# Kernel optimization log

Hardware: AMD Instinct MI355X
Metric: run time of the kernel (lower is better)

## Reference

```python
import jax, jax.numpy as jnp
import numpy as np

B, C, H, W = 2, 128, 64, 64
D_STATE, D_CONV, EXPAND = 16, 4, 2
D_INNER = EXPAND * C
DT_RANK = (C + 15) // 16  # ceil(d_model/16) = 8


def layernorm(x, w, b):
    # WithBias_LayerNorm over last (channel) dim, unbiased=False variance
    mu = jnp.mean(x, axis=-1, keepdims=True)
    var = jnp.mean((x - mu) ** 2, axis=-1, keepdims=True)
    return (x - mu) / jnp.sqrt(var + 1e-5) * w + b


def causal_conv1d_silu(x, w, b):
    # x: (b, d, l); w: (d, k) depthwise; causal pad k-1 on left, then SiLU
    k = w.shape[1]
    out = jax.lax.conv_general_dilated(
        x, w[:, None, :], window_strides=(1,), padding=[(k - 1, 0)],
        dimension_numbers=('NCH', 'OIH', 'NCH'), feature_group_count=w.shape[0])
    return jax.nn.silu(out + b[:, None])


def selective_scan(dA, dBu, Cm):
    # dA, dBu: (b, d, l, n); Cm: (b, n, l) -> y: (b, d, l)
    dA_t = jnp.moveaxis(dA, 2, 0)    # (l, b, d, n)
    dBu_t = jnp.moveaxis(dBu, 2, 0)  # (l, b, d, n)
    C_t = jnp.moveaxis(Cm, 2, 0)     # (l, b, n)

    def step(h, inp):
        a, bu, c = inp
        h = a * h + bu
        y = jnp.einsum('bdn,bn->bd', h, c)
        return h, y

    h0 = jnp.zeros(dA.shape[:2] + (dA.shape[3],), dA.dtype)
    _, ys = jax.lax.scan(step, h0, (dA_t, dBu_t, C_t))
    return jnp.moveaxis(ys, 0, 2)  # (b, d, l)


def mamba_branch(x3, W_in, W_z, conv_w, conv_b, W_x, W_dt, b_dt, A, D, W_out):
    # x3: (b, l, d_model) normalized input
    x = jnp.einsum('bld,ed->bel', x3, W_in)  # (b, d_inner, l)
    z = jnp.einsum('bld,ed->bel', x3, W_z)
    x = causal_conv1d_silu(x, conv_w, conv_b)
    xdbl = jnp.einsum('bdl,ed->bel', x, W_x)  # (b, dt_rank+2n, l)
    dt_low = xdbl[:, :DT_RANK]
    Bm = xdbl[:, DT_RANK:DT_RANK + D_STATE]
    Cm = xdbl[:, DT_RANK + D_STATE:]
    delta = jax.nn.softplus(jnp.einsum('brl,dr->bdl', dt_low, W_dt) + b_dt[:, None])
    dA = jnp.exp(delta[:, :, :, None] * A[None, :, None, :])           # (b,d,l,n)
    dBu = jnp.einsum('bdl,bnl->bdln', delta * x, Bm)                    # (b,d,l,n)
    y = selective_scan(dA, dBu, Cm)
    y = y + D[:, None] * x
    y = y * jax.nn.silu(z)
    return jnp.einsum('bdl,od->blo', y, W_out)  # (b, l, d_model)


def setup_inputs() -> dict:
    key = jax.random.key(0)
    ks = jax.random.split(key, 24)
    rn = lambda k, shp, s: jax.random.normal(k, shp, dtype=jnp.float32) * s
    inp = {}
    inp['pan'] = rn(ks[0], (B, C, H, W), 1.0)
    inp['ms'] = rn(ks[1], (B, C, H, W), 1.0)
    inp['norm_w_pan'] = jnp.ones((C,), jnp.float32)
    inp['norm_b_pan'] = jnp.zeros((C,), jnp.float32)
    inp['norm_w_ms'] = jnp.ones((C,), jnp.float32)
    inp['norm_b_ms'] = jnp.zeros((C,), jnp.float32)
    inp['W_in_pan'] = rn(ks[2], (D_INNER, C), C ** -0.5)
    inp['W_in_ms'] = rn(ks[3], (D_INNER, C), C ** -0.5)
    inp['W_z_pan'] = rn(ks[4], (D_INNER, C), C ** -0.5)
    inp['W_z_ms'] = rn(ks[5], (D_INNER, C), C ** -0.5)
    inp['conv_w_pan'] = rn(ks[6], (D_INNER, D_CONV), D_CONV ** -0.5)
    inp['conv_b_pan'] = rn(ks[7], (D_INNER,), 0.02)
    inp['conv_w_ms'] = rn(ks[8], (D_INNER, D_CONV), D_CONV ** -0.5)
    inp['conv_b_ms'] = rn(ks[9], (D_INNER,), 0.02)
    inp['W_x_pan'] = rn(ks[10], (DT_RANK + 2 * D_STATE, D_INNER), D_INNER ** -0.5)
    inp['W_x_ms'] = rn(ks[11], (DT_RANK + 2 * D_STATE, D_INNER), D_INNER ** -0.5)
    dt_std = DT_RANK ** -0.5
    inp['W_dt_pan'] = jax.random.uniform(ks[12], (D_INNER, DT_RANK), jnp.float32, -dt_std, dt_std)
    inp['W_dt_ms'] = jax.random.uniform(ks[13], (D_INNER, DT_RANK), jnp.float32, -dt_std, dt_std)
    # dt bias init: inverse-softplus of dt ~ logU[1e-3, 1e-1]
    u = np.asarray(jax.random.uniform(ks[14], (D_INNER,)))
    dt = np.exp(u * (np.log(0.1) - np.log(0.001)) + np.log(0.001)).clip(min=1e-4)
    inv_dt = dt + np.log(-np.expm1(-dt))
    inp['b_dt_pan'] = jnp.asarray(inv_dt, jnp.float32)
    inp['b_dt_ms'] = jnp.asarray(inv_dt, jnp.float32)
    inp['A_log'] = jnp.log(jnp.broadcast_to(jnp.arange(1, D_STATE + 1, dtype=jnp.float32), (D_INNER, D_STATE)))
    inp['D_pan'] = jnp.ones((D_INNER,), jnp.float32)
    inp['D_ms'] = jnp.ones((D_INNER,), jnp.float32)
    inp['W_out_pan'] = rn(ks[15], (C, D_INNER), D_INNER ** -0.5)
    inp['W_out_ms'] = rn(ks[16], (C, D_INNER), D_INNER ** -0.5)
    return inp


def reference(pan, ms, norm_w_pan, norm_b_pan, norm_w_ms, norm_b_ms,
              W_in_pan, W_in_ms, W_z_pan, W_z_ms,
              conv_w_pan, conv_b_pan, conv_w_ms, conv_b_ms,
              W_x_pan, W_x_ms, W_dt_pan, W_dt_ms, b_dt_pan, b_dt_ms,
              A_log, D_pan, D_ms, W_out_pan, W_out_ms):
    b, c, h, w = pan.shape
    A = -jnp.exp(A_log)
    pan3 = layernorm(pan.reshape(b, c, h * w).transpose(0, 2, 1), norm_w_pan, norm_b_pan)
    ms3 = layernorm(ms.reshape(b, c, h * w).transpose(0, 2, 1), norm_w_ms, norm_b_ms)
    out_pan = mamba_branch(pan3, W_in_pan, W_z_pan, conv_w_pan, conv_b_pan,
                           W_x_pan, W_dt_pan, b_dt_pan, A, D_pan, W_out_pan)
    out_ms = mamba_branch(ms3, W_in_ms, W_z_ms, conv_w_ms, conv_b_ms,
                          W_x_ms, W_dt_ms, b_dt_ms, A, D_ms, W_out_ms)
    out_pan = out_pan.transpose(0, 2, 1).reshape(b, c, h, w)
    out_ms = out_ms.transpose(0, 2, 1).reshape(b, c, h, w)
    return (out_pan, out_ms)
```

## Files before the change

### kernel.cpp

```cpp
#include <hip/hip_runtime.h>
#include <hip/hip_bf16.h>

constexpr int BB = 2;
constexpr int CC = 128;
constexpr int LL = 4096;
constexpr int DI = 256;
constexpr int DS = 16;
constexpr int DR = 8;
constexpr int DX = 40;
constexpr int NZ = 2 * BB;
constexpr int CH = 8;
constexpr int NCH = LL / CH;
constexpr int SEG = 32;

typedef short bf16x8 __attribute__((ext_vector_type(8)));
typedef float f32x4 __attribute__((ext_vector_type(4)));
typedef float f32x2 __attribute__((ext_vector_type(2)));

__device__ __forceinline__ unsigned short f2bf(float x) {
    __hip_bfloat16 h = __float2bfloat16(x);
    return *(unsigned short*)&h;
}
__device__ __forceinline__ float bflo(unsigned u) { return __uint_as_float(u << 16); }
__device__ __forceinline__ float bfhi(unsigned u) { return __uint_as_float(u & 0xffff0000u); }
__device__ __forceinline__ float bfu(unsigned short u) { return __uint_as_float((unsigned)u << 16); }
__device__ __forceinline__ float fast_rcp(float x) { return __builtin_amdgcn_rcpf(x); }
__device__ __forceinline__ float siluf(float x) { return x * fast_rcp(1.f + __expf(-x)); }
__device__ __forceinline__ float softplusf(float x) {
    const float z = exp2f(x * 1.44269504f);
    return (x > 20.f) ? x : 0.69314718f * log2f(1.f + z);
}

__global__ __launch_bounds__(256) void prep_kernel(
    const float* __restrict__ pan, const float* __restrict__ ms,
    const float* __restrict__ wpan, const float* __restrict__ bpan,
    const float* __restrict__ wms, const float* __restrict__ bms,
    const float* __restrict__ Winp, const float* __restrict__ Winm,
    const float* __restrict__ Wzp, const float* __restrict__ Wzm,
    const float* __restrict__ Woutp, const float* __restrict__ Woutm,
    const float* __restrict__ Wxp, const float* __restrict__ Wxm,
    unsigned short* __restrict__ x3b, unsigned short* __restrict__ wb)
{
    const int bx = blockIdx.x;
    const int t = threadIdx.x;
    if (bx >= 256) {
        const int i = (bx - 256) * 256 + t;
        const float* src; int off;
        if (i < 32768)       { src = Winp;  off = i; }
        else if (i < 65536)  { src = Winm;  off = i - 32768; }
        else if (i < 98304)  { src = Wzp;   off = i - 65536; }
        else if (i < 131072) { src = Wzm;   off = i - 98304; }
        else if (i < 163840) { src = Woutp; off = i - 131072; }
        else if (i < 196608) { src = Woutm; off = i - 163840; }
        else if (i < 206848) { src = Wxp;   off = i - 196608; }
        else                 { src = Wxm;   off = i - 206848; }
        wb[i] = f2bf(src[off]);
        return;
    }
    const int zi = bx >> 6;
    const int br = zi >> 1, b = zi & 1;
    const float* inp = br ? ms : pan;
    const float* wp = br ? wms : wpan;
    const float* bp = br ? bms : bpan;
    const int l0 = (bx & 63) * 64;
    const int lo = t & 63, c4 = t >> 6;
    const float* base = inp + (size_t)b * CC * LL + l0 + lo;
    float vals[32];
    float s = 0.f, s2 = 0.f;
    #pragma unroll
    for (int i = 0; i < 32; i++) {
        const int c = c4 * 32 + i;
        const float v = base[(size_t)c * LL];
        vals[i] = v; s += v; s2 += v * v;
    }
    __shared__ float red[2][4][64];
    red[0][c4][lo] = s; red[1][c4][lo] = s2;
    __syncthreads();
    const float S  = red[0][0][lo] + red[0][1][lo] + red[0][2][lo] + red[0][3][lo];
    const float S2 = red[1][0][lo] + red[1][1][lo] + red[1][2][lo] + red[1][3][lo];
    const float mu = S * (1.f / CC);
    const float var = S2 * (1.f / CC) - mu * mu;
    const float rstd = rsqrtf(var + 1e-5f);
    unsigned short* out = x3b + (size_t)zi * CC * LL + l0 + lo;
    #pragma unroll
    for (int i = 0; i < 32; i++) {
        const int c = c4 * 32 + i;
        out[(size_t)c * LL] = f2bf((vals[i] - mu) * rstd * wp[c] + bp[c]);
    }
}

__global__ __launch_bounds__(256) void gemm_inz_mfma(
    const unsigned short* __restrict__ wb, const unsigned short* __restrict__ x3b,
    unsigned short* __restrict__ xpre16, unsigned short* __restrict__ zb16)
{
    const int zi = blockIdx.z;
    const int my = blockIdx.y;
    const unsigned short* WI = wb + (zi >= BB ? 32768 : 0);
    const unsigned short* WZ = WI + 65536;
    const int mbase = my * 64;
    const unsigned short* Xb = x3b + (size_t)zi * CC * LL;
    const int n0 = blockIdx.x * 64;
    const int t = threadIdx.x;
    const int w = t >> 6, ln = t & 63;
    const int nf = ln & 15, qb = ln >> 4;
    bf16x8 afragI[4], afragZ[4];
    const int mrow = mbase + w * 16 + nf;
    #pragma unroll
    for (int c = 0; c < 4; c++) {
        afragI[c] = *(const bf16x8*)(WI + (size_t)mrow * CC + c * 32 + qb * 8);
        afragZ[c] = *(const bf16x8*)(WZ + (size_t)mrow * CC + c * 32 + qb * 8);
    }
    __shared__ unsigned short Bs[64][40];
    unsigned* Bw = (unsigned*)Bs;
    f32x4 accI[4] = {}, accZ[4] = {};
    const int kp = t >> 4, n4 = (t & 15) * 4;
    ushort4 a0 = *(const ushort4*)(Xb + (size_t)(2 * kp) * LL + n0 + n4);
    ushort4 a1 = *(const ushort4*)(Xb + (size_t)(2 * kp + 1) * LL + n0 + n4);
    #pragma unroll
    for (int kc = 0; kc < 4; kc++) {
        if (kc) __syncthreads();
        Bw[(n4 + 0) * 20 + kp] = (unsigned)a0.x | ((unsigned)a1.x << 16);
        Bw[(n4 + 1) * 20 + kp] = (unsigned)a0.y | ((unsigned)a1.y << 16);
        Bw[(n4 + 2) * 20 + kp] = (unsigned)a0.z | ((unsigned)a1.z << 16);
        Bw[(n4 + 3) * 20 + kp] = (unsigned)a0.w | ((unsigned)a1.w << 16);
        __syncthreads();
        if (kc < 3) {
            a0 = *(const ushort4*)(Xb + (size_t)((kc + 1) * 32 + 2 * kp) * LL + n0 + n4);
            a1 = *(const ushort4*)(Xb + (size_t)((kc + 1) * 32 + 2 * kp + 1) * LL + n0 + n4);
        }
        #pragma unroll
        for (int ns = 0; ns < 4; ns++) {
            const bf16x8 bf = *(const bf16x8*)(&Bs[ns * 16 + nf][qb * 8]);
            accI[ns] = __builtin_amdgcn_mfma_f32_16x16x32_bf16(afragI[kc], bf, accI[ns], 0, 0, 0);
            accZ[ns] = __builtin_amdgcn_mfma_f32_16x16x32_bf16(afragZ[kc], bf, accZ[ns], 0, 0, 0);
        }
    }
    #pragma unroll
    for (int ns = 0; ns < 4; ns++)
        #pragma unroll
        for (int r = 0; r < 4; r++) {
            const int m = mbase + w * 16 + qb * 4 + r;
            xpre16[((size_t)zi * DI + m) * LL + n0 + ns * 16 + nf] = f2bf(accI[ns][r]);
            zb16  [((size_t)zi * DI + m) * LL + n0 + ns * 16 + nf] = f2bf(accZ[ns][r]);
        }
}

__global__ __launch_bounds__(256) void gemm_x_mfma(
    const unsigned short* __restrict__ wb, const unsigned short* __restrict__ xpre16,
    const float* __restrict__ cw0, const float* __restrict__ cb0,
    const float* __restrict__ cw1, const float* __restrict__ cb1,
    unsigned short* __restrict__ xc, unsigned short* __restrict__ xdbl16)
{
    const int zi = blockIdx.z;
    const unsigned short* W = wb + 196608 + (zi >= BB ? 10240 : 0);
    const float* cw = (zi >= BB) ? cw1 : cw0;
    const float* cb = (zi >= BB) ? cb1 : cb0;
    const unsigned short* Xb = xpre16 + (size_t)zi * DI * LL;
    unsigned short* xcb = xc + (size_t)zi * DI * LL;
    const int n0 = blockIdx.x * 64;
    const int t = threadIdx.x;
    const int w = t >> 6, ln = t & 63;
    const int nf = ln & 15, qb = ln >> 4;
    bf16x8 zfrag;
    #pragma unroll
    for (int j = 0; j < 8; j++) zfrag[j] = 0;
    bf16x8 afrag[8];
    const int mrow = w * 16 + nf;
    #pragma unroll
    for (int c = 0; c < 8; c++)
        afrag[c] = (mrow < DX) ? *(const bf16x8*)(W + (size_t)mrow * DI + c * 32 + qb * 8) : zfrag;
    __shared__ unsigned short Bs[64][40];
    unsigned* Bw = (unsigned*)Bs;
    f32x4 acc[4] = {};
    const int kp = t >> 4, n4 = (t & 15) * 4;
    const bool edge = (n0 + n4 == 0);
    ushort4 cur0, cur1, prv0, prv1;
    {
        const unsigned short* xp0 = Xb + (size_t)(2 * kp) * LL + n0 + n4;
        const unsigned short* xp1 = Xb + (size_t)(2 * kp + 1) * LL + n0 + n4;
        cur0 = *(const ushort4*)xp0; cur1 = *(const ushort4*)xp1;
        if (!edge) { prv0 = *(const ushort4*)(xp0 - 4); prv1 = *(const ushort4*)(xp1 - 4); }
        else { prv0 = ushort4{0,0,0,0}; prv1 = ushort4{0,0,0,0}; }
    }
    #pragma unroll
    for (int kc = 0; kc < 8; kc++) {
        ushort4 o[2];
        #pragma unroll
        for (int rr = 0; rr < 2; rr++) {
            const int e = kc * 32 + 2 * kp + rr;
            const ushort4 cur = rr ? cur1 : cur0;
            const ushort4 prv = rr ? prv1 : prv0;
            const float xm3 = bfu(prv.y), xm2 = bfu(prv.z), xm1 = bfu(prv.w);
            const float c0 = bfu(cur.x), c1 = bfu(cur.y);
            const float c2 = bfu(cur.z), c3 = bfu(cur.w);
            const float w0 = cw[e * 4 + 0], w1 = cw[e * 4 + 1];
            const float w2 = cw[e * 4 + 2], w3 = cw[e * 4 + 3];
            const float bias = cb[e];
            o[rr].x = f2bf(siluf(w0 * xm3 + w1 * xm2 + w2 * xm1 + w3 * c0 + bias));
            o[rr].y = f2bf(siluf(w0 * xm2 + w1 * xm1 + w2 * c0 + w3 * c1 + bias));
            o[rr].z = f2bf(siluf(w0 * xm1 + w1 * c0 + w2 * c1 + w3 * c2 + bias));
            o[rr].w = f2bf(siluf(w0 * c0 + w1 * c1 + w2 * c2 + w3 * c3 + bias));
        }
        *(ushort4*)(xcb + (size_t)(kc * 32 + 2 * kp) * LL + n0 + n4) = o[0];
        *(ushort4*)(xcb + (size_t)(kc * 32 + 2 * kp + 1) * LL + n0 + n4) = o[1];
        if (kc) __syncthreads();
        Bw[(n4 + 0) * 20 + kp] = (unsigned)(unsigned short)o[0].x | ((unsigned)(unsigned short)o[1].x << 16);
        Bw[(n4 + 1) * 20 + kp] = (unsigned)(unsigned short)o[0].y | ((unsigned)(unsigned short)o[1].y << 16);
        Bw[(n4 + 2) * 20 + kp] = (unsigned)(unsigned short)o[0].z | ((unsigned)(unsigned short)o[1].z << 16);
        Bw[(n4 + 3) * 20 + kp] = (unsigned)(unsigned short)o[0].w | ((unsigned)(unsigned short)o[1].w << 16);
        __syncthreads();
        if (kc < 7) {
            const unsigned short* xp0 = Xb + (size_t)((kc + 1) * 32 + 2 * kp) * LL + n0 + n4;
            const unsigned short* xp1 = Xb + (size_t)((kc + 1) * 32 + 2 * kp + 1) * LL + n0 + n4;
            cur0 = *(const ushort4*)xp0; cur1 = *(const ushort4*)xp1;
            if (!edge) { prv0 = *(const ushort4*)(xp0 - 4); prv1 = *(const ushort4*)(xp1 - 4); }
        }
        #pragma unroll
        for (int ns = 0; ns < 4; ns++) {
            const bf16x8 bf = *(const bf16x8*)(&Bs[ns * 16 + nf][qb * 8]);
            acc[ns] = __builtin_amdgcn_mfma_f32_16x16x32_bf16(afrag[kc], bf, acc[ns], 0, 0, 0);
        }
    }
    #pragma unroll
    for (int ns = 0; ns < 4; ns++)
        #pragma unroll
        for (int r = 0; r < 4; r++) {
            const int m = w * 16 + qb * 4 + r;
            if (m < DX)
                xdbl16[((size_t)zi * DX + m) * LL + n0 + ns * 16 + nf] = f2bf(acc[ns][r]);
        }
}

__global__ __launch_bounds__(256) void gemm_out_mfma(
    const unsigned short* __restrict__ wb, const unsigned short* __restrict__ yb,
    float* __restrict__ outg)
{
    const int zi = blockIdx.z;
    const unsigned short* W = wb + 131072 + (zi >= BB ? 32768 : 0);
    const int mbase = blockIdx.y * 64;
    const unsigned short* Xb = yb + (size_t)zi * DI * LL;
    const int n0 = blockIdx.x * 64;
    const int t = threadIdx.x;
    const int w = t >> 6, ln = t & 63;
    const int nf = ln & 15, qb = ln >> 4;
    bf16x8 afrag[8];
    const int mrow = mbase + w * 16 + nf;
    #pragma unroll
    for (int c = 0; c < 8; c++)
        afrag[c] = *(const bf16x8*)(W + (size_t)mrow * DI + c * 32 + qb * 8);
    __shared__ unsigned short Bs[64][40];
    unsigned* Bw = (unsigned*)Bs;
    f32x4 acc[4] = {};
    const int kp = t >> 4, n4 = (t & 15) * 4;
    ushort4 a0 = *(const ushort4*)(Xb + (size_t)(2 * kp) * LL + n0 + n4);
    ushort4 a1 = *(const ushort4*)(Xb + (size_t)(2 * kp + 1) * LL + n0 + n4);
    #pragma unroll
    for (int kc = 0; kc < 8; kc++) {
        if (kc) __syncthreads();
        Bw[(n4 + 0) * 20 + kp] = (unsigned)a0.x | ((unsigned)a1.x << 16);
        Bw[(n4 + 1) * 20 + kp] = (unsigned)a0.y | ((unsigned)a1.y << 16);
        Bw[(n4 + 2) * 20 + kp] = (unsigned)a0.z | ((unsigned)a1.z << 16);
        Bw[(n4 + 3) * 20 + kp] = (unsigned)a0.w | ((unsigned)a1.w << 16);
        __syncthreads();
        if (kc < 7) {
            a0 = *(const ushort4*)(Xb + (size_t)((kc + 1) * 32 + 2 * kp) * LL + n0 + n4);
            a1 = *(const ushort4*)(Xb + (size_t)((kc + 1) * 32 + 2 * kp + 1) * LL + n0 + n4);
        }
        #pragma unroll
        for (int ns = 0; ns < 4; ns++) {
            const bf16x8 bf = *(const bf16x8*)(&Bs[ns * 16 + nf][qb * 8]);
            acc[ns] = __builtin_amdgcn_mfma_f32_16x16x32_bf16(afrag[kc], bf, acc[ns], 0, 0, 0);
        }
    }
    #pragma unroll
    for (int ns = 0; ns < 4; ns++)
        #pragma unroll
        for (int r = 0; r < 4; r++) {
            const int m = mbase + w * 16 + qb * 4 + r;
            outg[((size_t)zi * CC + m) * LL + n0 + ns * 16 + nf] = acc[ns][r];
        }
}

__global__ __launch_bounds__(512, 8) void scan_fused(
    const unsigned short* __restrict__ xc, const unsigned short* __restrict__ xdbl16,
    const float* __restrict__ A_log,
    const float* __restrict__ Wdt0, const float* __restrict__ Wdt1,
    const float* __restrict__ bdt0, const float* __restrict__ bdt1,
    const float* __restrict__ D0, const float* __restrict__ D1,
    const unsigned short* __restrict__ zb16, unsigned short* __restrict__ yb)
{
    const int blk = blockIdx.x;
    const int zi = blk >> 8;
    const int d  = blk & (DI - 1);
    const int t = threadIdx.x;
    const int l0 = t * CH;
    __shared__ float Ssh[DS * (NCH + 1)];
    __shared__ float sdl_sh[NCH];
    __shared__ float Pseg[DS * (SEG + 1)];
    __shared__ float Sseg[DS * (SEG + 1)];
    const unsigned short* xdb = xdbl16 + (size_t)zi * DX * LL;
    const float* Wdt = (zi >= BB) ? Wdt1 : Wdt0;
    const float* bdt = (zi >= BB) ? bdt1 : bdt0;
    const float dbias = bdt[d];
    float rx[CH];
    {
        const uint4 xv4 = *(const uint4*)(xc + (size_t)blk * LL + l0);
        rx[0] = bflo(xv4.x); rx[1] = bfhi(xv4.x);
        rx[2] = bflo(xv4.y); rx[3] = bfhi(xv4.y);
        rx[4] = bflo(xv4.z); rx[5] = bfhi(xv4.z);
        rx[6] = bflo(xv4.w); rx[7] = bfhi(xv4.w);
    }
    float e[CH], rdlx[CH];
    {
        f32x2 acc2[4];
        #pragma unroll
        for (int j = 0; j < 4; j++) acc2[j] = f32x2{dbias, dbias};
        #pragma unroll
        for (int r = 0; r < DR; r++) {
            const float wr = Wdt[d * DR + r];
            const f32x2 w2 = {wr, wr};
            const uint4 v = *(const uint4*)(xdb + (size_t)r * LL + l0);
            acc2[0] = w2 * f32x2{bflo(v.x), bfhi(v.x)} + acc2[0];
            acc2[1] = w2 * f32x2{bflo(v.y), bfhi(v.y)} + acc2[1];
            acc2[2] = w2 * f32x2{bflo(v.z), bfhi(v.z)} + acc2[2];
            acc2[3] = w2 * f32x2{bflo(v.w), bfhi(v.w)} + acc2[3];
        }
        float av[CH];
        av[0] = acc2[0].x; av[1] = acc2[0].y; av[2] = acc2[1].x; av[3] = acc2[1].y;
        av[4] = acc2[2].x; av[5] = acc2[2].y; av[6] = acc2[3].x; av[7] = acc2[3].y;
        float sdl = 0.f;
        #pragma unroll
        for (int i = 0; i < CH; i++) {
            const float sp = softplusf(av[i]);
            sdl += sp;
            rdlx[i] = sp * rx[i];
            e[i] = __expf(-sp);
        }
        sdl_sh[t] = sdl;
    }
    bool fast = true;
    #pragma unroll
    for (int n = 0; n < DS; n++)
        fast = fast && (fabsf(__expf(A_log[d * DS + n]) - (float)(n + 1)) < 1e-3f);
    const unsigned short* Bbase = xdb + (size_t)DR * LL;
    const unsigned short* Cbase = Bbase + (size_t)DS * LL;
    float y[CH];
    const int n2 = t & 15, sg = t >> 4;

    if (fast) {
        f32x2 e2[4], rdlx2[4];
        #pragma unroll
        for (int j = 0; j < 4; j++) {
            e2[j] = f32x2{e[2 * j], e[2 * j + 1]};
            rdlx2[j] = f32x2{rdlx[2 * j], rdlx[2 * j + 1]};
        }
        f32x2 pw2[4];
        #pragma unroll
        for (int j = 0; j < 4; j++) pw2[j] = f32x2{1.f, 1.f};
        #pragma unroll 4
        for (int n = 0; n < DS; n++) {
            const uint4 bv = *(const uint4*)(Bbase + (size_t)n * LL + l0);
            const f32x2 b0 = {bflo(bv.x), bfhi(bv.x)};
            const f32x2 b1 = {bflo(bv.y), bfhi(bv.y)};
            const f32x2 b2 = {bflo(bv.z), bfhi(bv.z)};
            const f32x2 b3 = {bflo(bv.w), bfhi(bv.w)};
            pw2[0] *= e2[0]; pw2[1] *= e2[1]; pw2[2] *= e2[2]; pw2[3] *= e2[3];
            const f32x2 u0 = rdlx2[0] * b0, u1 = rdlx2[1] * b1;
            const f32x2 u2 = rdlx2[2] * b2, u3 = rdlx2[3] * b3;
            float hn = u0.x;
            hn = fmaf(pw2[0].y, hn, u0.y);
            hn = fmaf(pw2[1].x, hn, u1.x);
            hn = fmaf(pw2[1].y, hn, u1.y);
            hn = fmaf(pw2[2].x, hn, u2.x);
            hn = fmaf(pw2[2].y, hn, u2.y);
            hn = fmaf(pw2[3].x, hn, u3.x);
            hn = fmaf(pw2[3].y, hn, u3.y);
            Ssh[n * (NCH + 1) + t] = hn;
        }
        __syncthreads();
        {
            const float Ann = -(float)(n2 + 1);
            float P = 1.f, S = 0.f;
            #pragma unroll
            for (int k = 0; k < 16; k++) {
                const int c = sg * 16 + k;
                const float p = __expf(Ann * sdl_sh[c]);
                const float s = Ssh[n2 * (NCH + 1) + c];
                S = fmaf(p, S, s);
                P *= p;
            }
            Pseg[n2 * (SEG + 1) + sg] = P;
            Sseg[n2 * (SEG + 1) + sg] = S;
        }
        __syncthreads();
        if (t < DS) {
            float h = 0.f;
            #pragma unroll 4
            for (int c2 = 0; c2 < SEG; c2++) {
                const float p = Pseg[t * (SEG + 1) + c2];
                const float s = Sseg[t * (SEG + 1) + c2];
                Sseg[t * (SEG + 1) + c2] = h;
                h = fmaf(p, h, s);
            }
        }
        __syncthreads();
        {
            const float Ann = -(float)(n2 + 1);
            float h = Sseg[n2 * (SEG + 1) + sg];
            #pragma unroll
            for (int k = 0; k < 16; k++) {
                const int c = sg * 16 + k;
                const float p = __expf(Ann * sdl_sh[c]);
                const float s = Ssh[n2 * (NCH + 1) + c];
                Ssh[n2 * (NCH + 1) + c] = h;
                h = fmaf(p, h, s);
            }
        }
        __syncthreads();
        f32x2 y2[4];
        #pragma unroll
        for (int j = 0; j < 4; j++) { y2[j] = f32x2{0.f, 0.f}; pw2[j] = f32x2{1.f, 1.f}; }
        #pragma unroll 2
        for (int n = 0; n < DS; n++) {
            const uint4 bv = *(const uint4*)(Bbase + (size_t)n * LL + l0);
            const uint4 cv = *(const uint4*)(Cbase + (size_t)n * LL + l0);
            const f32x2 b0 = {bflo(bv.x), bfhi(bv.x)};
            const f32x2 b1 = {bflo(bv.y), bfhi(bv.y)};
            const f32x2 b2 = {bflo(bv.z), bfhi(bv.z)};
            const f32x2 b3 = {bflo(bv.w), bfhi(bv.w)};
            const f32x2 c0 = {bflo(cv.x), bfhi(cv.x)};
            const f32x2 c1 = {bflo(cv.y), bfhi(cv.y)};
            const f32x2 c2 = {bflo(cv.z), bfhi(cv.z)};
            const f32x2 c3 = {bflo(cv.w), bfhi(cv.w)};
            pw2[0] *= e2[0]; pw2[1] *= e2[1]; pw2[2] *= e2[2]; pw2[3] *= e2[3];
            const f32x2 u0 = rdlx2[0] * b0, u1 = rdlx2[1] * b1;
            const f32x2 u2 = rdlx2[2] * b2, u3 = rdlx2[3] * b3;
            const float hp = Ssh[n * (NCH + 1) + t];
            const float h0 = fmaf(pw2[0].x, hp, u0.x);
            const float h1 = fmaf(pw2[0].y, h0, u0.y);
            y2[0] = f32x2{h0, h1} * c0 + y2[0];
            const float h2 = fmaf(pw2[1].x, h1, u1.x);
            const float h3 = fmaf(pw2[1].y, h2, u1.y);
            y2[1] = f32x2{h2, h3} * c1 + y2[1];
            const float h4 = fmaf(pw2[2].x, h3, u2.x);
            const float h5 = fmaf(pw2[2].y, h4, u2.y);
            y2[2] = f32x2{h4, h5} * c2 + y2[2];
            const float h6 = fmaf(pw2[3].x, h5, u3.x);
            const float h7 = fmaf(pw2[3].y, h6, u3.y);
            y2[3] = f32x2{h6, h7} * c3 + y2[3];
        }
        y[0] = y2[0].x; y[1] = y2[0].y; y[2] = y2[1].x; y[3] = y2[1].y;
        y[4] = y2[2].x; y[5] = y2[2].y; y[6] = y2[3].x; y[7] = y2[3].y;
    } else {
        float rdl[CH];
        #pragma unroll
        for (int i = 0; i < CH; i++) rdl[i] = -0.69314718f * log2f(e[i]);
        #pragma unroll 2
        for (int n = 0; n < DS; n++) {
            const float An = -__expf(A_log[d * DS + n]);
            const uint4 bv = *(const uint4*)(Bbase + (size_t)n * LL + l0);
            float hn = 0.f;
            hn = fmaf(__expf(rdl[0] * An), hn, rdlx[0] * bflo(bv.x));
            hn = fmaf(__expf(rdl[1] * An), hn, rdlx[1] * bfhi(bv.x));
            hn = fmaf(__expf(rdl[2] * An), hn, rdlx[2] * bflo(bv.y));
            hn = fmaf(__expf(rdl[3] * An), hn, rdlx[3] * bfhi(bv.y));
            hn = fmaf(__expf(rdl[4] * An), hn, rdlx[4] * bflo(bv.z));
            hn = fmaf(__expf(rdl[5] * An), hn, rdlx[5] * bfhi(bv.z));
            hn = fmaf(__expf(rdl[6] * An), hn, rdlx[6] * bflo(bv.w));
            hn = fmaf(__expf(rdl[7] * An), hn, rdlx[7] * bfhi(bv.w));
            Ssh[n * (NCH + 1) + t] = hn;
        }
        __syncthreads();
        {
            const float Ann = -__expf(A_log[d * DS + n2]);
            float P = 1.f, S = 0.f;
            #pragma unroll
            for (int k = 0; k < 16; k++) {
                const int c = sg * 16 + k;
                const float p = __expf(Ann * sdl_sh[c]);
                const float s = Ssh[n2 * (NCH + 1) + c];
                S = fmaf(p, S, s);
                P *= p;
            }
            Pseg[n2 * (SEG + 1) + sg] = P;
            Sseg[n2 * (SEG + 1) + sg] = S;
        }
        __syncthreads();
        if (t < DS) {
            float h = 0.f;
            #pragma unroll 4
            for (int c2 = 0; c2 < SEG; c2++) {
                const float p = Pseg[t * (SEG + 1) + c2];
                const float s = Sseg[t * (SEG + 1) + c2];
                Sseg[t * (SEG + 1) + c2] = h;
                h = fmaf(p, h, s);
            }
        }
        __syncthreads();
        {
            const float Ann = -__expf(A_log[d * DS + n2]);
            float h = Sseg[n2 * (SEG + 1) + sg];
            #pragma unroll
            for (int k = 0; k < 16; k++) {
                const int c = sg * 16 + k;
                const float p = __expf(Ann * sdl_sh[c]);
                const float s = Ssh[n2 * (NCH + 1) + c];
                Ssh[n2 * (NCH + 1) + c] = h;
                h = fmaf(p, h, s);
            }
        }
        __syncthreads();
        #pragma unroll
        for (int i = 0; i < CH; i++) y[i] = 0.f;
        #pragma unroll 2
        for (int n = 0; n < DS; n++) {
            const float An = -__expf(A_log[d * DS + n]);
            const uint4 bv = *(const uint4*)(Bbase + (size_t)n * LL + l0);
            const uint4 cv = *(const uint4*)(Cbase + (size_t)n * LL + l0);
            float hn = Ssh[n * (NCH + 1) + t];
            hn = fmaf(__expf(rdl[0] * An), hn, rdlx[0] * bflo(bv.x)); y[0] = fmaf(hn, bflo(cv.x), y[0]);
            hn = fmaf(__expf(rdl[1] * An), hn, rdlx[1] * bfhi(bv.x)); y[1] = fmaf(hn, bfhi(cv.x), y[1]);
            hn = fmaf(__expf(rdl[2] * An), hn, rdlx[2] * bflo(bv.y)); y[2] = fmaf(hn, bflo(cv.y), y[2]);
            hn = fmaf(__expf(rdl[3] * An), hn, rdlx[3] * bfhi(bv.y)); y[3] = fmaf(hn, bfhi(cv.y), y[3]);
            hn = fmaf(__expf(rdl[4] * An), hn, rdlx[4] * bflo(bv.z)); y[4] = fmaf(hn, bflo(cv.z), y[4]);
            hn = fmaf(__expf(rdl[5] * An), hn, rdlx[5] * bfhi(bv.z)); y[5] = fmaf(hn, bfhi(cv.z), y[5]);
            hn = fmaf(__expf(rdl[6] * An), hn, rdlx[6] * bflo(bv.w)); y[6] = fmaf(hn, bflo(cv.w), y[6]);
            hn = fmaf(__expf(rdl[7] * An), hn, rdlx[7] * bfhi(bv.w)); y[7] = fmaf(hn, bfhi(cv.w), y[7]);
        }
    }
    const float Dd = ((zi >= BB) ? D1 : D0)[d];
    const unsigned short* z_g = zb16 + (size_t)blk * LL + l0;
    unsigned short* y_g = yb + (size_t)blk * LL + l0;
    {
        const uint4 zv = *(const uint4*)z_g;
        float zf[CH];
        zf[0] = bflo(zv.x); zf[1] = bfhi(zv.x); zf[2] = bflo(zv.y); zf[3] = bfhi(zv.y);
        zf[4] = bflo(zv.z); zf[5] = bfhi(zv.z); zf[6] = bflo(zv.w); zf[7] = bfhi(zv.w);
        ushort4 r0, r1;
        #pragma unroll
        for (int i = 0; i < CH; i++) {
            const float val = (y[i] + Dd * rx[i]) * siluf(zf[i]);
            if (i < 4) ((unsigned short*)&r0)[i] = f2bf(val);
            else       ((unsigned short*)&r1)[i - 4] = f2bf(val);
        }
        *(ushort4*)(y_g + 0) = r0;
        *(ushort4*)(y_g + 4) = r1;
    }
}

extern "C" void kernel_launch(void* const* d_in, const int* in_sizes, int n_in,
                              void* d_out, int out_size, void* d_ws, size_t ws_size,
                              hipStream_t stream)
{
    (void)in_sizes; (void)n_in; (void)out_size; (void)ws_size;
    auto fp = [&](int i) { return (const float*)d_in[i]; };
    const float *pan = fp(0), *ms = fp(1);
    const float *nwp = fp(2), *nbp = fp(3), *nwm = fp(4), *nbm = fp(5);
    const float *Winp = fp(6), *Winm = fp(7), *Wzp = fp(8), *Wzm = fp(9);
    const float *cwp = fp(10), *cbp = fp(11), *cwm = fp(12), *cbm = fp(13);
    const float *Wxp = fp(14), *Wxm = fp(15);
    const float *Wdtp = fp(16), *Wdtm = fp(17), *bdtp = fp(18), *bdtm = fp(19);
    const float *Alog = fp(20), *Dp = fp(21), *Dm = fp(22);
    const float *Woutp = fp(23), *Woutm = fp(24);

    unsigned short* us = (unsigned short*)d_ws;
    unsigned short* x3b    = us;
    unsigned short* xpre16 = x3b    + (size_t)NZ * CC * LL;
    unsigned short* zb16   = xpre16 + (size_t)NZ * DI * LL;
    unsigned short* xdbl16 = zb16   + (size_t)NZ * DI * LL;
    unsigned short* yb     = xdbl16 + (size_t)NZ * DX * LL;
    unsigned short* xc     = yb     + (size_t)NZ * DI * LL;
    unsigned short* wb     = xc     + (size_t)NZ * DI * LL;
    float* out = (float*)d_out;

    prep_kernel<<<dim3(256 + 848), 256, 0, stream>>>(
        pan, ms, nwp, nbp, nwm, nbm,
        Winp, Winm, Wzp, Wzm, Woutp, Woutm, Wxp, Wxm, x3b, wb);
    gemm_inz_mfma<<<dim3(LL / 64, 4, NZ), 256, 0, stream>>>(wb, x3b, xpre16, zb16);
    gemm_x_mfma<<<dim3(LL / 64, 1, NZ), 256, 0, stream>>>(wb, xpre16, cwp, cbp, cwm, cbm, xc, xdbl16);
    scan_fused<<<dim3(NZ * DI), 512, 0, stream>>>(xc, xdbl16, Alog, Wdtp, Wdtm, bdtp, bdtm,
                                                  Dp, Dm, zb16, yb);
    gemm_out_mfma<<<dim3(LL / 64, 2, NZ), 256, 0, stream>>>(wb, yb, out);
}
```

Measured before the change: 167.8 us.

## Fuse layernorm and weight conversion into GEMMs, drop prep kernel

Removes the separate prep kernel. Layernorm is now computed inside the in/z GEMM, and the fp32 weights are converted to bf16 on the fly inside each GEMM. The SiLU on z moves into the GEMM epilogue, and the scan caches its per-chunk decay exponentials instead of recomputing them. This saves a launch and the x3b round trip through memory, at the cost of each of the 4 M-tile blocks redundantly recomputing layernorm statistics and reloading fp32 weights. It also stores silu(z) in bf16 rather than z itself.

```diff
diff --git a/kernel.cpp b/kernel.cpp
--- a/kernel.cpp
+++ b/kernel.cpp
@@ -30,104 +30,102 @@
     const float z = exp2f(x * 1.44269504f);
     return (x > 20.f) ? x : 0.69314718f * log2f(1.f + z);
 }
-
-__global__ __launch_bounds__(256) void prep_kernel(
+__device__ __forceinline__ unsigned pk2(float lo, float hi) {
+    return (unsigned)f2bf(lo) | ((unsigned)f2bf(hi) << 16);
+}
+__device__ __forceinline__ bf16x8 cvt8(const float4 a, const float4 b) {
+    bf16x8 r;
+    r[0] = (short)f2bf(a.x); r[1] = (short)f2bf(a.y);
+    r[2] = (short)f2bf(a.z); r[3] = (short)f2bf(a.w);
+    r[4] = (short)f2bf(b.x); r[5] = (short)f2bf(b.y);
+    r[6] = (short)f2bf(b.z); r[7] = (short)f2bf(b.w);
+    return r;
+}
+
+__global__ __launch_bounds__(256) void gemm_inz_mfma(
     const float* __restrict__ pan, const float* __restrict__ ms,
     const float* __restrict__ wpan, const float* __restrict__ bpan,
     const float* __restrict__ wms, const float* __restrict__ bms,
     const float* __restrict__ Winp, const float* __restrict__ Winm,
     const float* __restrict__ Wzp, const float* __restrict__ Wzm,
-    const float* __restrict__ Woutp, const float* __restrict__ Woutm,
-    const float* __restrict__ Wxp, const float* __restrict__ Wxm,
-    unsigned short* __restrict__ x3b, unsigned short* __restrict__ wb)
-{
-    const int bx = blockIdx.x;
-    const int t = threadIdx.x;
-    if (bx >= 256) {
-        const int i = (bx - 256) * 256 + t;
-        const float* src; int off;
-        if (i < 32768)       { src = Winp;  off = i; }
-        else if (i < 65536)  { src = Winm;  off = i - 32768; }
-        else if (i < 98304)  { src = Wzp;   off = i - 65536; }
-        else if (i < 131072) { src = Wzm;   off = i - 98304; }
-        else if (i < 163840) { src = Woutp; off = i - 131072; }
-        else if (i < 196608) { src = Woutm; off = i - 163840; }
-        else if (i < 206848) { src = Wxp;   off = i - 196608; }
-        else                 { src = Wxm;   off = i - 206848; }
-        wb[i] = f2bf(src[off]);
-        return;
-    }
-    const int zi = bx >> 6;
-    const int br = zi >> 1, b = zi & 1;
-    const float* inp = br ? ms : pan;
-    const float* wp = br ? wms : wpan;
-    const float* bp = br ? bms : bpan;
-    const int l0 = (bx & 63) * 64;
-    const int lo = t & 63, c4 = t >> 6;
-    const float* base = inp + (size_t)b * CC * LL + l0 + lo;
-    float vals[32];
-    float s = 0.f, s2 = 0.f;
-    #pragma unroll
-    for (int i = 0; i < 32; i++) {
-        const int c = c4 * 32 + i;
-        const float v = base[(size_t)c * LL];
-        vals[i] = v; s += v; s2 += v * v;
-    }
-    __shared__ float red[2][4][64];
-    red[0][c4][lo] = s; red[1][c4][lo] = s2;
-    __syncthreads();
-    const float S  = red[0][0][lo] + red[0][1][lo] + red[0][2][lo] + red[0][3][lo];
-    const float S2 = red[1][0][lo] + red[1][1][lo] + red[1][2][lo] + red[1][3][lo];
-    const float mu = S * (1.f / CC);
-    const float var = S2 * (1.f / CC) - mu * mu;
-    const float rstd = rsqrtf(var + 1e-5f);
-    unsigned short* out = x3b + (size_t)zi * CC * LL + l0 + lo;
-    #pragma unroll
-    for (int i = 0; i < 32; i++) {
-        const int c = c4 * 32 + i;
-        out[(size_t)c * LL] = f2bf((vals[i] - mu) * rstd * wp[c] + bp[c]);
-    }
-}
-
-__global__ __launch_bounds__(256) void gemm_inz_mfma(
-    const unsigned short* __restrict__ wb, const unsigned short* __restrict__ x3b,
     unsigned short* __restrict__ xpre16, unsigned short* __restrict__ zb16)
 {
     const int zi = blockIdx.z;
     const int my = blockIdx.y;
-    const unsigned short* WI = wb + (zi >= BB ? 32768 : 0);
-    const unsigned short* WZ = WI + 65536;
+    const bool br = (zi >= BB);
+    const float* WIf = br ? Winm : Winp;
+    const float* WZf = br ? Wzm : Wzp;
+    const float* inp = br ? ms : pan;
+    const float* wln = br ? wms : wpan;
+    const float* bln = br ? bms : bpan;
     const int mbase = my * 64;
-    const unsigned short* Xb = x3b + (size_t)zi * CC * LL;
     const int n0 = blockIdx.x * 64;
     const int t = threadIdx.x;
     const int w = t >> 6, ln = t & 63;
     const int nf = ln & 15, qb = ln >> 4;
+    const int kp = t >> 4, n4 = (t & 15) * 4;
+
     bf16x8 afragI[4], afragZ[4];
     const int mrow = mbase + w * 16 + nf;
     #pragma unroll
     for (int c = 0; c < 4; c++) {
-        afragI[c] = *(const bf16x8*)(WI + (size_t)mrow * CC + c * 32 + qb * 8);
-        afragZ[c] = *(const bf16x8*)(WZ + (size_t)mrow * CC + c * 32 + qb * 8);
-    }
+        const float* pi = WIf + (size_t)mrow * CC + c * 32 + qb * 8;
+        const float* pz = WZf + (size_t)mrow * CC + c * 32 + qb * 8;
+        afragI[c] = cvt8(*(const float4*)pi, *(const float4*)(pi + 4));
+        afragZ[c] = cvt8(*(const float4*)pz, *(const float4*)(pz + 4));
+    }
+
+    const float* xbase = inp + (size_t)(zi & 1) * CC * LL + n0 + n4;
+    float xv[8][4];
+    float wrow[8], brow[8];
+    float sm[4] = {}, sq[4] = {};
+    #pragma unroll
+    for (int j = 0; j < 8; j++) {
+        const int r = (j >> 1) * 32 + 2 * kp + (j & 1);
+        const float4 v = *(const float4*)(xbase + (size_t)r * LL);
+        xv[j][0] = v.x; xv[j][1] = v.y; xv[j][2] = v.z; xv[j][3] = v.w;
+        wrow[j] = wln[r]; brow[j] = bln[r];
+        sm[0] += v.x; sm[1] += v.y; sm[2] += v.z; sm[3] += v.w;
+        sq[0] += v.x * v.x; sq[1] += v.y * v.y; sq[2] += v.z * v.z; sq[3] += v.w * v.w;
+    }
+    __shared__ float redS[16][64];
+    __shared__ float redQ[16][64];
+    #pragma unroll
+    for (int j = 0; j < 4; j++) { redS[kp][n4 + j] = sm[j]; redQ[kp][n4 + j] = sq[j]; }
+    __syncthreads();
+    float mu[4], rs[4];
+    #pragma unroll
+    for (int j = 0; j < 4; j++) { sm[j] = 0.f; sq[j] = 0.f; }
+    #pragma unroll
+    for (int k = 0; k < 16; k++)
+        #pragma unroll
+        for (int j = 0; j < 4; j++) { sm[j] += redS[k][n4 + j]; sq[j] += redQ[k][n4 + j]; }
+    #pragma unroll
+    for (int j = 0; j < 4; j++) {
+        mu[j] = sm[j] * (1.f / CC);
+        rs[j] = rsqrtf(sq[j] * (1.f / CC) - mu[j] * mu[j] + 1e-5f);
+    }
+    unsigned pk[4][4];
+    #pragma unroll
+    for (int kc = 0; kc < 4; kc++)
+        #pragma unroll
+        for (int j = 0; j < 4; j++) {
+            const float lo = (xv[kc * 2 + 0][j] - mu[j]) * rs[j] * wrow[kc * 2 + 0] + brow[kc * 2 + 0];
+            const float hi = (xv[kc * 2 + 1][j] - mu[j]) * rs[j] * wrow[kc * 2 + 1] + brow[kc * 2 + 1];
+            pk[kc][j] = pk2(lo, hi);
+        }
+
     __shared__ unsigned short Bs[64][40];
     unsigned* Bw = (unsigned*)Bs;
     f32x4 accI[4] = {}, accZ[4] = {};
-    const int kp = t >> 4, n4 = (t & 15) * 4;
-    ushort4 a0 = *(const ushort4*)(Xb + (size_t)(2 * kp) * LL + n0 + n4);
-    ushort4 a1 = *(const ushort4*)(Xb + (size_t)(2 * kp + 1) * LL + n0 + n4);
     #pragma unroll
     for (int kc = 0; kc < 4; kc++) {
         if (kc) __syncthreads();
-        Bw[(n4 + 0) * 20 + kp] = (unsigned)a0.x | ((unsigned)a1.x << 16);
-        Bw[(n4 + 1) * 20 + kp] = (unsigned)a0.y | ((unsigned)a1.y << 16);
-        Bw[(n4 + 2) * 20 + kp] = (unsigned)a0.z | ((unsigned)a1.z << 16);
-        Bw[(n4 + 3) * 20 + kp] = (unsigned)a0.w | ((unsigned)a1.w << 16);
-        __syncthreads();
-        if (kc < 3) {
-            a0 = *(const ushort4*)(Xb + (size_t)((kc + 1) * 32 + 2 * kp) * LL + n0 + n4);
-            a1 = *(const ushort4*)(Xb + (size_t)((kc + 1) * 32 + 2 * kp + 1) * LL + n0 + n4);
-        }
+        Bw[(n4 + 0) * 20 + kp] = pk[kc][0];
+        Bw[(n4 + 1) * 20 + kp] = pk[kc][1];
+        Bw[(n4 + 2) * 20 + kp] = pk[kc][2];
+        Bw[(n4 + 3) * 20 + kp] = pk[kc][3];
+        __syncthreads();
         #pragma unroll
         for (int ns = 0; ns < 4; ns++) {
             const bf16x8 bf = *(const bf16x8*)(&Bs[ns * 16 + nf][qb * 8]);
@@ -141,18 +139,19 @@
         for (int r = 0; r < 4; r++) {
             const int m = mbase + w * 16 + qb * 4 + r;
             xpre16[((size_t)zi * DI + m) * LL + n0 + ns * 16 + nf] = f2bf(accI[ns][r]);
-            zb16  [((size_t)zi * DI + m) * LL + n0 + ns * 16 + nf] = f2bf(accZ[ns][r]);
+            zb16  [((size_t)zi * DI + m) * LL + n0 + ns * 16 + nf] = f2bf(siluf(accZ[ns][r]));
         }
 }
 
 __global__ __launch_bounds__(256) void gemm_x_mfma(
-    const unsigned short* __restrict__ wb, const unsigned short* __restrict__ xpre16,
+    const float* __restrict__ Wxp, const float* __restrict__ Wxm,
+    const unsigned short* __restrict__ xpre16,
     const float* __restrict__ cw0, const float* __restrict__ cb0,
     const float* __restrict__ cw1, const float* __restrict__ cb1,
     unsigned short* __restrict__ xc, unsigned short* __restrict__ xdbl16)
 {
     const int zi = blockIdx.z;
-    const unsigned short* W = wb + 196608 + (zi >= BB ? 10240 : 0);
+    const float* Wf = (zi >= BB) ? Wxm : Wxp;
     const float* cw = (zi >= BB) ? cw1 : cw0;
     const float* cb = (zi >= BB) ? cb1 : cb0;
     const unsigned short* Xb = xpre16 + (size_t)zi * DI * LL;
@@ -167,8 +166,12 @@
     bf16x8 afrag[8];
     const int mrow = w * 16 + nf;
     #pragma unroll
-    for (int c = 0; c < 8; c++)
-        afrag[c] = (mrow < DX) ? *(const bf16x8*)(W + (size_t)mrow * DI + c * 32 + qb * 8) : zfrag;
+    for (int c = 0; c < 8; c++) {
+        if (mrow < DX) {
+            const float* p = Wf + (size_t)mrow * DI + c * 32 + qb * 8;
+            afrag[c] = cvt8(*(const float4*)p, *(const float4*)(p + 4));
+        } else afrag[c] = zfrag;
+    }
     __shared__ unsigned short Bs[64][40];
     unsigned* Bw = (unsigned*)Bs;
     f32x4 acc[4] = {};
@@ -232,11 +235,11 @@
 }
 
 __global__ __launch_bounds__(256) void gemm_out_mfma(
-    const unsigned short* __restrict__ wb, const unsigned short* __restrict__ yb,
-    float* __restrict__ outg)
+    const float* __restrict__ Woutp, const float* __restrict__ Woutm,
+    const unsigned short* __restrict__ yb, float* __restrict__ outg)
 {
     const int zi = blockIdx.z;
-    const unsigned short* W = wb + 131072 + (zi >= BB ? 32768 : 0);
+    const float* Wf = (zi >= BB) ? Woutm : Woutp;
     const int mbase = blockIdx.y * 64;
     const unsigned short* Xb = yb + (size_t)zi * DI * LL;
     const int n0 = blockIdx.x * 64;
@@ -246,8 +249,10 @@
     bf16x8 afrag[8];
     const int mrow = mbase + w * 16 + nf;
     #pragma unroll
-    for (int c = 0; c < 8; c++)
-        afrag[c] = *(const bf16x8*)(W + (size_t)mrow * DI + c * 32 + qb * 8);
+    for (int c = 0; c < 8; c++) {
+        const float* p = Wf + (size_t)mrow * DI + c * 32 + qb * 8;
+        afrag[c] = cvt8(*(const float4*)p, *(const float4*)(p + 4));
+    }
     __shared__ unsigned short Bs[64][40];
     unsigned* Bw = (unsigned*)Bs;
     f32x4 acc[4] = {};
@@ -378,6 +383,7 @@
             Ssh[n * (NCH + 1) + t] = hn;
         }
         __syncthreads();
+        float pcache[16];
         {
             const float Ann = -(float)(n2 + 1);
             float P = 1.f, S = 0.f;
@@ -385,6 +391,7 @@
             for (int k = 0; k < 16; k++) {
                 const int c = sg * 16 + k;
                 const float p = __expf(Ann * sdl_sh[c]);
+                pcache[k] = p;
                 const float s = Ssh[n2 * (NCH + 1) + c];
                 S = fmaf(p, S, s);
                 P *= p;
@@ -405,22 +412,20 @@
         }
         __syncthreads();
         {
-            const float Ann = -(float)(n2 + 1);
             float h = Sseg[n2 * (SEG + 1) + sg];
             #pragma unroll
             for (int k = 0; k < 16; k++) {
                 const int c = sg * 16 + k;
-                const float p = __expf(Ann * sdl_sh[c]);
                 const float s = Ssh[n2 * (NCH + 1) + c];
                 Ssh[n2 * (NCH + 1) + c] = h;
-                h = fmaf(p, h, s);
+                h = fmaf(pcache[k], h, s);
             }
         }
         __syncthreads();
         f32x2 y2[4];
         #pragma unroll
         for (int j = 0; j < 4; j++) { y2[j] = f32x2{0.f, 0.f}; pw2[j] = f32x2{1.f, 1.f}; }
-        #pragma unroll 2
+        #pragma unroll 4
         for (int n = 0; n < DS; n++) {
             const uint4 bv = *(const uint4*)(Bbase + (size_t)n * LL + l0);
             const uint4 cv = *(const uint4*)(Cbase + (size_t)n * LL + l0);
@@ -539,7 +544,7 @@
         ushort4 r0, r1;
         #pragma unroll
         for (int i = 0; i < CH; i++) {
-            const float val = (y[i] + Dd * rx[i]) * siluf(zf[i]);
+            const float val = (y[i] + Dd * rx[i]) * zf[i];
             if (i < 4) ((unsigned short*)&r0)[i] = f2bf(val);
             else       ((unsigned short*)&r1)[i - 4] = f2bf(val);
         }
@@ -564,21 +569,18 @@
     const float *Woutp = fp(23), *Woutm = fp(24);
 
     unsigned short* us = (unsigned short*)d_ws;
-    unsigned short* x3b    = us;
-    unsigned short* xpre16 = x3b    + (size_t)NZ * CC * LL;
+    unsigned short* xpre16 = us;
     unsigned short* zb16   = xpre16 + (size_t)NZ * DI * LL;
     unsigned short* xdbl16 = zb16   + (size_t)NZ * DI * LL;
     unsigned short* yb     = xdbl16 + (size_t)NZ * DX * LL;
     unsigned short* xc     = yb     + (size_t)NZ * DI * LL;
-    unsigned short* wb     = xc     + (size_t)NZ * DI * LL;
     float* out = (float*)d_out;
 
-    prep_kernel<<<dim3(256 + 848), 256, 0, stream>>>(
-        pan, ms, nwp, nbp, nwm, nbm,
-        Winp, Winm, Wzp, Wzm, Woutp, Woutm, Wxp, Wxm, x3b, wb);
-    gemm_inz_mfma<<<dim3(LL / 64, 4, NZ), 256, 0, stream>>>(wb, x3b, xpre16, zb16);
-    gemm_x_mfma<<<dim3(LL / 64, 1, NZ), 256, 0, stream>>>(wb, xpre16, cwp, cbp, cwm, cbm, xc, xdbl16);
+    gemm_inz_mfma<<<dim3(LL / 64, 4, NZ), 256, 0, stream>>>(
+        pan, ms, nwp, nbp, nwm, nbm, Winp, Winm, Wzp, Wzm, xpre16, zb16);
+    gemm_x_mfma<<<dim3(LL / 64, 1, NZ), 256, 0, stream>>>(
+        Wxp, Wxm, xpre16, cwp, cbp, cwm, cbm, xc, xdbl16);
     scan_fused<<<dim3(NZ * DI), 512, 0, stream>>>(xc, xdbl16, Alog, Wdtp, Wdtm, bdtp, bdtm,
                                                   Dp, Dm, zb16, yb);
-    gemm_out_mfma<<<dim3(LL / 64, 2, NZ), 256, 0, stream>>>(wb, yb, out);
-}
+    gemm_out_mfma<<<dim3(LL / 64, 2, NZ), 256, 0, stream>>>(Woutp, Woutm, yb, out);
+}
```

After: 178.2 us. +6.2%, slower.
